# Kernel tuning notes

Hardware: AMD Instinct MI355X
Metric: run time of the kernel (lower is better)

## Reference

```python
import jax, jax.numpy as jnp
import numpy as np

B, T, C, H = 8, 2048, 1024, 128  # batch, seq, n_embed, head_size


def setup_inputs() -> dict:
    key = jax.random.key(0)
    ks = jax.random.split(key, 7)
    s = 1.0 / np.sqrt(C)
    return {
        "x": jax.random.normal(ks[0], (B, T, C), dtype=jnp.float32),
        "Wq": jax.random.uniform(ks[1], (C, H), jnp.float32, -s, s),
        "bq": jax.random.uniform(ks[2], (H,), jnp.float32, -s, s),
        "Wk": jax.random.uniform(ks[3], (C, H), jnp.float32, -s, s),
        "bk": jax.random.uniform(ks[4], (H,), jnp.float32, -s, s),
        "Wv": jax.random.uniform(ks[5], (C, H), jnp.float32, -s, s),
        "bv": jax.random.uniform(ks[6], (H,), jnp.float32, -s, s),
    }


def reference(x, Wq, bq, Wk, bk, Wv, bv):
    # Projections: [B, T, H]
    Q = jnp.einsum("btc,ch->bth", x, Wq) + bq
    K = jnp.einsum("btc,ch->bth", x, Wk) + bk
    V = jnp.einsum("btc,ch->bth", x, Wv) + bv
    # Scores scaled by n_embed**-0.5 (faithful to source, which uses C not head_size)
    scale = jnp.asarray(C, x.dtype) ** -0.5
    scores = jnp.einsum("bqh,bkh->bqk", Q, K) * scale  # [B, T, T]
    causal = jnp.tril(jnp.ones((T, T), dtype=bool))
    scores = jnp.where(causal, scores, jnp.asarray(-jnp.inf, x.dtype))
    attn = jax.nn.softmax(scores, axis=-1)
    # dropout p=0.0 (eval) -> identity
    return jnp.einsum("bqk,bkh->bqh", attn, V)
```

## Files before the change

kernel.cpp:

```cpp
#include <hip/hip_runtime.h>
#include <hip/hip_bf16.h>
#include <math.h>

typedef __attribute__((ext_vector_type(4))) float f32x4;
typedef __attribute__((ext_vector_type(8))) short s16x8;
typedef __attribute__((ext_vector_type(4))) short s16x4;

#define NB 8
#define NT 2048
#define NC 1024
#define NH 128
#define QSCALE 0.04508422002778f

__device__ __forceinline__ short f2bf(float f) {
  union { float f; unsigned u; } v; v.f = f;
  unsigned r = v.u + 0x7fffu + ((v.u >> 16) & 1u);
  return (short)(r >> 16);
}

__global__ void wt_kernel(const float* __restrict__ Wq, const float* __restrict__ Wk,
                          const float* __restrict__ Wv, short* __restrict__ Wt) {
  int idx = blockIdx.x * 256 + threadIdx.x;
  if (idx >= 3 * 128 * 1024) return;
  int m = idx >> 17;
  int n = (idx >> 10) & 127;
  int k = idx & 1023;
  const float* W = (m == 0) ? Wq : ((m == 1) ? Wk : Wv);
  Wt[idx] = f2bf(W[k * 128 + n]);
}

#define PK_PAD 72
#define PT_PAD 136

__global__ __launch_bounds__(256)
void proj_kernel(const float* __restrict__ x, const short* __restrict__ Wt,
                 const float* __restrict__ bq, const float* __restrict__ bk,
                 const float* __restrict__ bv,
                 short* __restrict__ Qb, short* __restrict__ Kb, short* __restrict__ Vtb) {
  __shared__ __align__(16) char smem[2 * 128 * PK_PAD * 2];
  short* Ax = (short*)smem;
  short* Bw = (short*)(smem + 128 * PK_PAD * 2);
  short* Tr = (short*)smem;

  const int tid = threadIdx.x;
  const int m0 = blockIdx.x * 128;
  const int proj = blockIdx.y;
  const int w = tid >> 6, lane = tid & 63;
  const int lr = lane & 15, lg = lane >> 4;

  f32x4 acc[2][8];
#pragma unroll
  for (int i = 0; i < 2; i++)
#pragma unroll
    for (int j = 0; j < 8; j++) acc[i][j] = {0.f, 0.f, 0.f, 0.f};

  const short* Wtp = Wt + proj * (128 * 1024);

  for (int k0 = 0; k0 < NC; k0 += 64) {
#pragma unroll
    for (int i = 0; i < 4; i++) {
      int idx = tid + 256 * i;
      int row = idx >> 3, c8 = idx & 7;
      const float* src = x + (size_t)(m0 + row) * NC + k0 + c8 * 8;
      float4 a = *(const float4*)src;
      float4 b = *(const float4*)(src + 4);
      s16x8 v;
      v[0] = f2bf(a.x); v[1] = f2bf(a.y); v[2] = f2bf(a.z); v[3] = f2bf(a.w);
      v[4] = f2bf(b.x); v[5] = f2bf(b.y); v[6] = f2bf(b.z); v[7] = f2bf(b.w);
      *(s16x8*)(Ax + row * PK_PAD + c8 * 8) = v;
    }
#pragma unroll
    for (int i = 0; i < 4; i++) {
      int idx = tid + 256 * i;
      int n = idx >> 3, c8 = idx & 7;
      s16x8 v = *(const s16x8*)(Wtp + n * 1024 + k0 + c8 * 8);
      *(s16x8*)(Bw + n * PK_PAD + c8 * 8) = v;
    }
    __syncthreads();
#pragma unroll
    for (int kc = 0; kc < 2; kc++) {
      s16x8 af[2];
#pragma unroll
      for (int mi = 0; mi < 2; mi++) {
        int row = w * 32 + mi * 16 + lr;
        af[mi] = *(const s16x8*)(Ax + row * PK_PAD + kc * 32 + lg * 8);
      }
#pragma unroll
      for (int ni = 0; ni < 8; ni++) {
        s16x8 bf = *(const s16x8*)(Bw + (ni * 16 + lr) * PK_PAD + kc * 32 + lg * 8);
        acc[0][ni] = __builtin_amdgcn_mfma_f32_16x16x32_bf16(af[0], bf, acc[0][ni], 0, 0, 0);
        acc[1][ni] = __builtin_amdgcn_mfma_f32_16x16x32_bf16(af[1], bf, acc[1][ni], 0, 0, 0);
      }
    }
    __syncthreads();
  }

  const float* bias = (proj == 0) ? bq : ((proj == 1) ? bk : bv);
  const float scl = (proj == 0) ? QSCALE : 1.0f;

  if (proj < 2) {
#pragma unroll
    for (int mi = 0; mi < 2; mi++)
#pragma unroll
      for (int ni = 0; ni < 8; ni++) {
        float bn = bias[ni * 16 + lr];
#pragma unroll
        for (int r = 0; r < 4; r++) {
          int t = w * 32 + mi * 16 + lg * 4 + r;
          Tr[t * PT_PAD + ni * 16 + lr] = f2bf((acc[mi][ni][r] + bn) * scl);
        }
      }
    __syncthreads();
    short* dst = (proj == 0) ? Qb : Kb;
#pragma unroll
    for (int i = 0; i < 8; i++) {
      int c = tid + 256 * i;
      int t = c >> 4, c8 = c & 15;
      s16x8 v = *(const s16x8*)(Tr + t * PT_PAD + c8 * 8);
      *(s16x8*)(dst + (size_t)(m0 + t) * NH + c8 * 8) = v;
    }
  } else {
#pragma unroll
    for (int mi = 0; mi < 2; mi++)
#pragma unroll
      for (int ni = 0; ni < 8; ni++) {
        float bn = bias[ni * 16 + lr];
        int d = ni * 16 + lr;
        int t = w * 32 + mi * 16 + lg * 4;
        s16x4 v;
        v[0] = f2bf(acc[mi][ni][0] + bn);
        v[1] = f2bf(acc[mi][ni][1] + bn);
        v[2] = f2bf(acc[mi][ni][2] + bn);
        v[3] = f2bf(acc[mi][ni][3] + bn);
        *(s16x4*)(Tr + d * PT_PAD + t) = v;
      }
    __syncthreads();
    int b = m0 >> 11;
    int tb = m0 & 2047;
#pragma unroll
    for (int i = 0; i < 8; i++) {
      int c = tid + 256 * i;
      int d = c >> 4, c8 = c & 15;
      s16x8 v = *(const s16x8*)(Tr + d * PT_PAD + c8 * 8);
      *(s16x8*)(Vtb + (size_t)b * (NH * NT) + (size_t)d * NT + tb + c8 * 8) = v;
    }
  }
}

#define KPAD 136
#define VPAD 72

__global__ __launch_bounds__(128)
void attn_kernel(const short* __restrict__ Qb, const short* __restrict__ Kb,
                 const short* __restrict__ Vtb, float* __restrict__ out) {
  __shared__ __align__(16) short Kl[64 * KPAD];
  __shared__ __align__(16) short Vl[128 * VPAD];

  const int tid = threadIdx.x;
  const int w = tid >> 6, lane = tid & 63;
  const int lr = lane & 15, lg = lane >> 4;

  const int bid = blockIdx.x;
  const int batch = bid >> 6;
  const int qtile = 63 - (bid & 63);
  const int q0 = qtile * 32;

  const int qrow = q0 + w * 16 + lr;
  const short* Qrow = Qb + (size_t)(batch * NT + qrow) * NH;
  s16x8 qf[4];
#pragma unroll
  for (int dc = 0; dc < 4; dc++) qf[dc] = *(const s16x8*)(Qrow + dc * 32 + lg * 8);

  f32x4 acc[8];
#pragma unroll
  for (int i = 0; i < 8; i++) acc[i] = {0.f, 0.f, 0.f, 0.f};
  float m_run = -3.0e38f, l_run = 0.f;

  const int ntiles = (q0 + 95) >> 6;
  const short* Kbase = Kb + (size_t)batch * NT * NH;
  const short* Vbase = Vtb + (size_t)batch * NH * NT;

  for (int it = 0; it < ntiles; it++) {
    const int kv0 = it * 64;
#pragma unroll
    for (int i = 0; i < 8; i++) {
      int idx = tid + 128 * i;
      int row = idx >> 4, c8 = idx & 15;
      s16x8 v = *(const s16x8*)(Kbase + (size_t)(kv0 + row) * NH + c8 * 8);
      *(s16x8*)(Kl + row * KPAD + c8 * 8) = v;
    }
#pragma unroll
    for (int i = 0; i < 8; i++) {
      int idx = tid + 128 * i;
      int d = idx >> 3, c8 = idx & 7;
      s16x8 v = *(const s16x8*)(Vbase + (size_t)d * NT + kv0 + c8 * 8);
      *(s16x8*)(Vl + d * VPAD + c8 * 8) = v;
    }
    __syncthreads();

    f32x4 st[4];
#pragma unroll
    for (int km = 0; km < 4; km++) st[km] = {0.f, 0.f, 0.f, 0.f};
#pragma unroll
    for (int dc = 0; dc < 4; dc++)
#pragma unroll
      for (int km = 0; km < 4; km++) {
        s16x8 kf = *(const s16x8*)(Kl + (km * 16 + lr) * KPAD + dc * 32 + lg * 8);
        st[km] = __builtin_amdgcn_mfma_f32_16x16x32_bf16(kf, qf[dc], st[km], 0, 0, 0);
      }

    if (kv0 + 63 > q0) {
#pragma unroll
      for (int km = 0; km < 4; km++)
#pragma unroll
        for (int r = 0; r < 4; r++) {
          int kg = kv0 + km * 16 + lg * 4 + r;
          if (kg > qrow) st[km][r] = -3.0e38f;
        }
    }

    float tm = -3.0e38f;
#pragma unroll
    for (int km = 0; km < 4; km++)
#pragma unroll
      for (int r = 0; r < 4; r++) tm = fmaxf(tm, st[km][r]);
    tm = fmaxf(tm, __shfl_xor(tm, 16, 64));
    tm = fmaxf(tm, __shfl_xor(tm, 32, 64));
    float m_new = fmaxf(m_run, tm);
    float corr = exp2f(m_run - m_new);

    float psum = 0.f;
    s16x8 pf[2];
#pragma unroll
    for (int km = 0; km < 4; km++)
#pragma unroll
      for (int r = 0; r < 4; r++) {
        float p = exp2f(st[km][r] - m_new);
        psum += p;
        pf[km >> 1][(km & 1) * 4 + r] = f2bf(p);
      }
    psum += __shfl_xor(psum, 16, 64);
    psum += __shfl_xor(psum, 32, 64);
    l_run = l_run * corr + psum;
    m_run = m_new;
#pragma unroll
    for (int i = 0; i < 8; i++) acc[i] *= corr;

#pragma unroll
    for (int ks = 0; ks < 2; ks++)
#pragma unroll
      for (int dm = 0; dm < 8; dm++) {
        const short* vp = Vl + (dm * 16 + lr) * VPAD + ks * 32 + lg * 4;
        s16x4 v0 = *(const s16x4*)vp;
        s16x4 v1 = *(const s16x4*)(vp + 16);
        s16x8 vf = __builtin_shufflevector(v0, v1, 0, 1, 2, 3, 4, 5, 6, 7);
        acc[dm] = __builtin_amdgcn_mfma_f32_16x16x32_bf16(vf, pf[ks], acc[dm], 0, 0, 0);
      }
    __syncthreads();
  }

  const float inv = 1.f / l_run;
  float* orow = out + (size_t)(batch * NT + qrow) * NH;
#pragma unroll
  for (int dm = 0; dm < 8; dm++) {
    float4 o;
    o.x = acc[dm][0] * inv;
    o.y = acc[dm][1] * inv;
    o.z = acc[dm][2] * inv;
    o.w = acc[dm][3] * inv;
    *(float4*)(orow + dm * 16 + lg * 4) = o;
  }
}

extern "C" void kernel_launch(void* const* d_in, const int* in_sizes, int n_in,
                              void* d_out, int out_size, void* d_ws, size_t ws_size,
                              hipStream_t stream) {
  const float* x = (const float*)d_in[0];
  const float* Wq = (const float*)d_in[1];
  const float* bq = (const float*)d_in[2];
  const float* Wk = (const float*)d_in[3];
  const float* bk = (const float*)d_in[4];
  const float* Wv = (const float*)d_in[5];
  const float* bv = (const float*)d_in[6];
  float* out = (float*)d_out;

  char* ws = (char*)d_ws;
  short* Wt = (short*)ws;
  short* Qb = (short*)(ws + 786432);
  short* Kb = (short*)(ws + 786432 + 4194304);
  short* Vtb = (short*)(ws + 786432 + 2 * 4194304);

  wt_kernel<<<dim3(1536), dim3(256), 0, stream>>>(Wq, Wk, Wv, Wt);
  proj_kernel<<<dim3(128, 3), dim3(256), 0, stream>>>(x, Wt, bq, bk, bv, Qb, Kb, Vtb);
  attn_kernel<<<dim3(512), dim3(128), 0, stream>>>(Qb, Kb, Vtb, out);
}
```

Before: 191.1 us.

## Rewrite all three kernels: tiled weight transpose, pipelined projection, split-KV attention

```diff
diff --git a/kernel.cpp b/kernel.cpp
--- a/kernel.cpp
+++ b/kernel.cpp
@@ -18,257 +18,284 @@
   return (short)(r >> 16);
 }
 
-__global__ void wt_kernel(const float* __restrict__ Wq, const float* __restrict__ Wk,
-                          const float* __restrict__ Wv, short* __restrict__ Wt) {
-  int idx = blockIdx.x * 256 + threadIdx.x;
-  if (idx >= 3 * 128 * 1024) return;
-  int m = idx >> 17;
-  int n = (idx >> 10) & 127;
-  int k = idx & 1023;
-  const float* W = (m == 0) ? Wq : ((m == 1) ? Wk : Wv);
-  Wt[idx] = f2bf(W[k * 128 + n]);
-}
-
-#define PK_PAD 72
-#define PT_PAD 136
+__device__ __forceinline__ void glds16(const short* g, short* l) {
+  __builtin_amdgcn_global_load_lds(
+      (const __attribute__((address_space(1))) unsigned int*)g,
+      (__attribute__((address_space(3))) unsigned int*)l, 16, 0, 0);
+}
 
 __global__ __launch_bounds__(256)
+void wt_kernel(const float* __restrict__ Wq, const float* __restrict__ Wk,
+               const float* __restrict__ Wv, short* __restrict__ Wt) {
+  __shared__ short T[64 * 72];
+  const int tid = threadIdx.x;
+  const int k0 = blockIdx.x * 64, n0 = blockIdx.y * 64, proj = blockIdx.z;
+  const float* W = (proj == 0) ? Wq : ((proj == 1) ? Wk : Wv);
+#pragma unroll
+  for (int u = 0; u < 4; u++) {
+    int row = u * 16 + (tid >> 4);
+    int col4 = (tid & 15) * 4;
+    float4 v = *(const float4*)(W + (size_t)(k0 + row) * NH + n0 + col4);
+    T[(col4 + 0) * 72 + row] = f2bf(v.x);
+    T[(col4 + 1) * 72 + row] = f2bf(v.y);
+    T[(col4 + 2) * 72 + row] = f2bf(v.z);
+    T[(col4 + 3) * 72 + row] = f2bf(v.w);
+  }
+  __syncthreads();
+#pragma unroll
+  for (int u = 0; u < 2; u++) {
+    int c = tid + 256 * u;
+    int n = c >> 3, c8 = c & 7;
+    s16x8 v = *(const s16x8*)(T + n * 72 + c8 * 8);
+    *(s16x8*)(Wt + (size_t)proj * (NH * NC) + (size_t)(n0 + n) * NC + k0 + c8 * 8) = v;
+  }
+}
+
+__global__ __launch_bounds__(256, 3)
 void proj_kernel(const float* __restrict__ x, const short* __restrict__ Wt,
                  const float* __restrict__ bq, const float* __restrict__ bk,
                  const float* __restrict__ bv,
                  short* __restrict__ Qb, short* __restrict__ Kb, short* __restrict__ Vtb) {
-  __shared__ __align__(16) char smem[2 * 128 * PK_PAD * 2];
-  short* Ax = (short*)smem;
-  short* Bw = (short*)(smem + 128 * PK_PAD * 2);
-  short* Tr = (short*)smem;
-
-  const int tid = threadIdx.x;
-  const int m0 = blockIdx.x * 128;
-  const int proj = blockIdx.y;
-  const int w = tid >> 6, lane = tid & 63;
-  const int lr = lane & 15, lg = lane >> 4;
-
-  f32x4 acc[2][8];
-#pragma unroll
-  for (int i = 0; i < 2; i++)
-#pragma unroll
-    for (int j = 0; j < 8; j++) acc[i][j] = {0.f, 0.f, 0.f, 0.f};
-
-  const short* Wtp = Wt + proj * (128 * 1024);
-
-  for (int k0 = 0; k0 < NC; k0 += 64) {
-#pragma unroll
-    for (int i = 0; i < 4; i++) {
-      int idx = tid + 256 * i;
-      int row = idx >> 3, c8 = idx & 7;
-      const float* src = x + (size_t)(m0 + row) * NC + k0 + c8 * 8;
-      float4 a = *(const float4*)src;
-      float4 b = *(const float4*)(src + 4);
-      s16x8 v;
-      v[0] = f2bf(a.x); v[1] = f2bf(a.y); v[2] = f2bf(a.z); v[3] = f2bf(a.w);
-      v[4] = f2bf(b.x); v[5] = f2bf(b.y); v[6] = f2bf(b.z); v[7] = f2bf(b.w);
-      *(s16x8*)(Ax + row * PK_PAD + c8 * 8) = v;
-    }
-#pragma unroll
-    for (int i = 0; i < 4; i++) {
-      int idx = tid + 256 * i;
-      int n = idx >> 3, c8 = idx & 7;
-      s16x8 v = *(const s16x8*)(Wtp + n * 1024 + k0 + c8 * 8);
-      *(s16x8*)(Bw + n * PK_PAD + c8 * 8) = v;
-    }
-    __syncthreads();
-#pragma unroll
-    for (int kc = 0; kc < 2; kc++) {
-      s16x8 af[2];
-#pragma unroll
-      for (int mi = 0; mi < 2; mi++) {
-        int row = w * 32 + mi * 16 + lr;
-        af[mi] = *(const s16x8*)(Ax + row * PK_PAD + kc * 32 + lg * 8);
-      }
-#pragma unroll
-      for (int ni = 0; ni < 8; ni++) {
-        s16x8 bf = *(const s16x8*)(Bw + (ni * 16 + lr) * PK_PAD + kc * 32 + lg * 8);
-        acc[0][ni] = __builtin_amdgcn_mfma_f32_16x16x32_bf16(af[0], bf, acc[0][ni], 0, 0, 0);
-        acc[1][ni] = __builtin_amdgcn_mfma_f32_16x16x32_bf16(af[1], bf, acc[1][ni], 0, 0, 0);
-      }
-    }
-    __syncthreads();
-  }
-
-  const float* bias = (proj == 0) ? bq : ((proj == 1) ? bk : bv);
-  const float scl = (proj == 0) ? QSCALE : 1.0f;
-
-  if (proj < 2) {
-#pragma unroll
-    for (int mi = 0; mi < 2; mi++)
-#pragma unroll
-      for (int ni = 0; ni < 8; ni++) {
-        float bn = bias[ni * 16 + lr];
-#pragma unroll
-        for (int r = 0; r < 4; r++) {
-          int t = w * 32 + mi * 16 + lg * 4 + r;
-          Tr[t * PT_PAD + ni * 16 + lr] = f2bf((acc[mi][ni][r] + bn) * scl);
-        }
-      }
-    __syncthreads();
-    short* dst = (proj == 0) ? Qb : Kb;
-#pragma unroll
-    for (int i = 0; i < 8; i++) {
-      int c = tid + 256 * i;
-      int t = c >> 4, c8 = c & 15;
-      s16x8 v = *(const s16x8*)(Tr + t * PT_PAD + c8 * 8);
-      *(s16x8*)(dst + (size_t)(m0 + t) * NH + c8 * 8) = v;
-    }
-  } else {
-#pragma unroll
-    for (int mi = 0; mi < 2; mi++)
-#pragma unroll
-      for (int ni = 0; ni < 8; ni++) {
-        float bn = bias[ni * 16 + lr];
-        int d = ni * 16 + lr;
-        int t = w * 32 + mi * 16 + lg * 4;
-        s16x4 v;
-        v[0] = f2bf(acc[mi][ni][0] + bn);
-        v[1] = f2bf(acc[mi][ni][1] + bn);
-        v[2] = f2bf(acc[mi][ni][2] + bn);
-        v[3] = f2bf(acc[mi][ni][3] + bn);
-        *(s16x4*)(Tr + d * PT_PAD + t) = v;
-      }
-    __syncthreads();
-    int b = m0 >> 11;
-    int tb = m0 & 2047;
-#pragma unroll
-    for (int i = 0; i < 8; i++) {
-      int c = tid + 256 * i;
-      int d = c >> 4, c8 = c & 15;
-      s16x8 v = *(const s16x8*)(Tr + d * PT_PAD + c8 * 8);
-      *(s16x8*)(Vtb + (size_t)b * (NH * NT) + (size_t)d * NT + tb + c8 * 8) = v;
-    }
-  }
-}
-
-#define KPAD 136
-#define VPAD 72
-
-__global__ __launch_bounds__(128)
-void attn_kernel(const short* __restrict__ Qb, const short* __restrict__ Kb,
-                 const short* __restrict__ Vtb, float* __restrict__ out) {
-  __shared__ __align__(16) short Kl[64 * KPAD];
-  __shared__ __align__(16) short Vl[128 * VPAD];
+  __shared__ __align__(16) short smem[2 * 12288];
 
   const int tid = threadIdx.x;
   const int w = tid >> 6, lane = tid & 63;
   const int lr = lane & 15, lg = lane >> 4;
 
   const int bid = blockIdx.x;
-  const int batch = bid >> 6;
-  const int qtile = 63 - (bid & 63);
-  const int q0 = qtile * 32;
-
-  const int qrow = q0 + w * 16 + lr;
-  const short* Qrow = Qb + (size_t)(batch * NT + qrow) * NH;
-  s16x8 qf[4];
-#pragma unroll
-  for (int dc = 0; dc < 4; dc++) qf[dc] = *(const s16x8*)(Qrow + dc * 32 + lg * 8);
+  const int orig = (bid & 7) * 96 + (bid >> 3);
+  const int proj = orig >> 8;
+  const int m0 = (orig & 255) * 64;
+
+  const short* Wtp = Wt + (size_t)proj * (NH * NC);
 
   f32x4 acc[8];
 #pragma unroll
   for (int i = 0; i < 8; i++) acc[i] = {0.f, 0.f, 0.f, 0.f};
-  float m_run = -3.0e38f, l_run = 0.f;
-
-  const int ntiles = (q0 + 95) >> 6;
-  const short* Kbase = Kb + (size_t)batch * NT * NH;
-  const short* Vbase = Vtb + (size_t)batch * NH * NT;
-
-  for (int it = 0; it < ntiles; it++) {
-    const int kv0 = it * 64;
-#pragma unroll
-    for (int i = 0; i < 8; i++) {
-      int idx = tid + 128 * i;
-      int row = idx >> 4, c8 = idx & 15;
-      s16x8 v = *(const s16x8*)(Kbase + (size_t)(kv0 + row) * NH + c8 * 8);
-      *(s16x8*)(Kl + row * KPAD + c8 * 8) = v;
-    }
-#pragma unroll
-    for (int i = 0; i < 8; i++) {
-      int idx = tid + 128 * i;
-      int d = idx >> 3, c8 = idx & 7;
-      s16x8 v = *(const s16x8*)(Vbase + (size_t)d * NT + kv0 + c8 * 8);
-      *(s16x8*)(Vl + d * VPAD + c8 * 8) = v;
-    }
-    __syncthreads();
-
-    f32x4 st[4];
-#pragma unroll
-    for (int km = 0; km < 4; km++) st[km] = {0.f, 0.f, 0.f, 0.f};
-#pragma unroll
-    for (int dc = 0; dc < 4; dc++)
-#pragma unroll
-      for (int km = 0; km < 4; km++) {
-        s16x8 kf = *(const s16x8*)(Kl + (km * 16 + lr) * KPAD + dc * 32 + lg * 8);
-        st[km] = __builtin_amdgcn_mfma_f32_16x16x32_bf16(kf, qf[dc], st[km], 0, 0, 0);
-      }
-
-    if (kv0 + 63 > q0) {
-#pragma unroll
-      for (int km = 0; km < 4; km++)
+
+  const int s0 = 2 * tid, s1 = 2 * tid + 1;
+  const int ar0 = s0 >> 3, ac0 = s0 & 7, ar1 = s1 >> 3, ac1 = s1 & 7;
+  const float* asrc0base = x + (size_t)(m0 + ar0) * NC + ((ac0 ^ (ar0 & 7)) * 8);
+  const float* asrc1base = x + (size_t)(m0 + ar1) * NC + ((ac1 ^ (ar1 & 7)) * 8);
+
+  float4 a00, a01, a10, a11;
+
+  auto stageA_load = [&](int k0) {
+    a00 = *(const float4*)(asrc0base + k0);
+    a01 = *(const float4*)(asrc0base + k0 + 4);
+    a10 = *(const float4*)(asrc1base + k0);
+    a11 = *(const float4*)(asrc1base + k0 + 4);
+  };
+  auto stageA_write = [&](int buf) {
+    s16x8 v;
+    v[0] = f2bf(a00.x); v[1] = f2bf(a00.y); v[2] = f2bf(a00.z); v[3] = f2bf(a00.w);
+    v[4] = f2bf(a01.x); v[5] = f2bf(a01.y); v[6] = f2bf(a01.z); v[7] = f2bf(a01.w);
+    *(s16x8*)(smem + buf * 12288 + s0 * 8) = v;
+    v[0] = f2bf(a10.x); v[1] = f2bf(a10.y); v[2] = f2bf(a10.z); v[3] = f2bf(a10.w);
+    v[4] = f2bf(a11.x); v[5] = f2bf(a11.y); v[6] = f2bf(a11.z); v[7] = f2bf(a11.w);
+    *(s16x8*)(smem + buf * 12288 + s1 * 8) = v;
+  };
+  auto stageB = [&](int buf, int k0) {
+#pragma unroll
+    for (int u = 0; u < 4; u++) {
+      int g = w * 4 + u;
+      int s = g * 64 + lane;
+      int n = s >> 3, c8 = s & 7;
+      const short* src = Wtp + (size_t)n * NC + k0 + ((c8 ^ (n & 7)) * 8);
+      short* dst = smem + buf * 12288 + 4096 + g * 512;
+      glds16(src, dst);
+    }
+  };
+
+  stageA_load(0);
+  stageB(0, 0);
+  stageA_write(0);
+  __syncthreads();
+
+  for (int it = 0; it < 16; ++it) {
+    int buf = it & 1, nb = buf ^ 1;
+    if (it < 15) { stageA_load((it + 1) * 64); stageB(nb, (it + 1) * 64); }
+    const short* A = smem + buf * 12288;
+    const short* B = smem + buf * 12288 + 4096;
+    const int arow = w * 16 + lr;
+#pragma unroll
+    for (int kc = 0; kc < 2; kc++) {
+      s16x8 af = *(const s16x8*)(A + arow * 64 + (((kc * 4 + lg) ^ (arow & 7)) * 8));
+#pragma unroll
+      for (int ni = 0; ni < 8; ni++) {
+        int brow = ni * 16 + lr;
+        s16x8 bf = *(const s16x8*)(B + brow * 64 + (((kc * 4 + lg) ^ (brow & 7)) * 8));
+        acc[ni] = __builtin_amdgcn_mfma_f32_16x16x32_bf16(af, bf, acc[ni], 0, 0, 0);
+      }
+    }
+    if (it < 15) stageA_write(nb);
+    __syncthreads();
+  }
+
+  const float* bias = (proj == 0) ? bq : ((proj == 1) ? bk : bv);
+  const float scl = (proj == 0) ? QSCALE : 1.0f;
+  short* Tr = smem;
+
+  if (proj < 2) {
+#pragma unroll
+    for (int ni = 0; ni < 8; ni++) {
+      float bn = bias[ni * 16 + lr];
+#pragma unroll
+      for (int r = 0; r < 4; r++) {
+        int t = w * 16 + lg * 4 + r;
+        Tr[t * 136 + ni * 16 + lr] = f2bf((acc[ni][r] + bn) * scl);
+      }
+    }
+    __syncthreads();
+    short* dst = (proj == 0) ? Qb : Kb;
+#pragma unroll
+    for (int i = 0; i < 4; i++) {
+      int c = tid + 256 * i;
+      int t = c >> 4, c8 = c & 15;
+      s16x8 v = *(const s16x8*)(Tr + t * 136 + c8 * 8);
+      *(s16x8*)(dst + (size_t)(m0 + t) * NH + c8 * 8) = v;
+    }
+  } else {
+#pragma unroll
+    for (int ni = 0; ni < 8; ni++) {
+      float bn = bias[ni * 16 + lr];
+      int d = ni * 16 + lr;
+      int t = w * 16 + lg * 4;
+      s16x4 v;
+      v[0] = f2bf(acc[ni][0] + bn);
+      v[1] = f2bf(acc[ni][1] + bn);
+      v[2] = f2bf(acc[ni][2] + bn);
+      v[3] = f2bf(acc[ni][3] + bn);
+      *(s16x4*)(Tr + d * 72 + t) = v;
+    }
+    __syncthreads();
+    int b = m0 >> 11, t0 = m0 & 2047;
+#pragma unroll
+    for (int i = 0; i < 4; i++) {
+      int c = tid + 256 * i;
+      int d = c >> 3, c8 = c & 7;
+      s16x8 v = *(const s16x8*)(Tr + d * 72 + c8 * 8);
+      *(s16x8*)(Vtb + (size_t)b * (NH * NT) + (size_t)d * NT + t0 + c8 * 8) = v;
+    }
+  }
+}
+
+__global__ __launch_bounds__(256, 3)
+void attn_kernel(const short* __restrict__ Qb, const short* __restrict__ Kb,
+                 const short* __restrict__ Vtb, float* __restrict__ out) {
+  __shared__ float Cb[3][16][132];
+  __shared__ float2 Ml[3][16];
+
+  const int tid = threadIdx.x;
+  const int w = tid >> 6, lane = tid & 63;
+  const int lr = lane & 15, lg = lane >> 4;
+
+  const int bid = blockIdx.x;
+  const int orig = (bid & 7) * 64 + (bid >> 3);
+  const int batch = orig >> 6;
+  const int pairid = orig & 63;
+
+  const short* Kp = Kb + (size_t)batch * NT * NH;
+  const short* Vp = Vtb + (size_t)batch * NH * NT;
+
+#pragma unroll 1
+  for (int ph = 0; ph < 2; ph++) {
+    const int j = ph ? (127 - pairid) : pairid;
+    const int q0 = j * 16;
+    const int q = q0 + lr;
+
+    const short* Qrow = Qb + (size_t)(batch * NT + q) * NH;
+    s16x8 qf[4];
+#pragma unroll
+    for (int dc = 0; dc < 4; dc++) qf[dc] = *(const s16x8*)(Qrow + dc * 32 + lg * 8);
+
+    f32x4 acc[8];
+#pragma unroll
+    for (int i = 0; i < 8; i++) acc[i] = {0.f, 0.f, 0.f, 0.f};
+    float m_run = -3.0e38f, l_run = 0.f;
+
+    const int Nt = (q0 + 47) >> 5;
+
+    for (int t = w; t < Nt; t += 4) {
+      const int kv0 = t * 32;
+      f32x4 st0 = {0.f, 0.f, 0.f, 0.f}, st1 = st0;
+      const short* Kt = Kp + (size_t)(kv0 + lr) * NH + lg * 8;
+#pragma unroll
+      for (int dc = 0; dc < 4; dc++) {
+        s16x8 k0f = *(const s16x8*)(Kt + dc * 32);
+        s16x8 k1f = *(const s16x8*)(Kt + 16 * NH + dc * 32);
+        st0 = __builtin_amdgcn_mfma_f32_16x16x32_bf16(k0f, qf[dc], st0, 0, 0, 0);
+        st1 = __builtin_amdgcn_mfma_f32_16x16x32_bf16(k1f, qf[dc], st1, 0, 0, 0);
+      }
+      if (kv0 + 31 > q0) {
 #pragma unroll
         for (int r = 0; r < 4; r++) {
-          int kg = kv0 + km * 16 + lg * 4 + r;
-          if (kg > qrow) st[km][r] = -3.0e38f;
+          if (kv0 + lg * 4 + r > q) st0[r] = -3.0e38f;
+          if (kv0 + 16 + lg * 4 + r > q) st1[r] = -3.0e38f;
         }
-    }
-
-    float tm = -3.0e38f;
-#pragma unroll
-    for (int km = 0; km < 4; km++)
-#pragma unroll
-      for (int r = 0; r < 4; r++) tm = fmaxf(tm, st[km][r]);
-    tm = fmaxf(tm, __shfl_xor(tm, 16, 64));
-    tm = fmaxf(tm, __shfl_xor(tm, 32, 64));
-    float m_new = fmaxf(m_run, tm);
-    float corr = exp2f(m_run - m_new);
-
-    float psum = 0.f;
-    s16x8 pf[2];
-#pragma unroll
-    for (int km = 0; km < 4; km++)
+      }
+      float tm = -3.0e38f;
+#pragma unroll
+      for (int r = 0; r < 4; r++) { tm = fmaxf(tm, st0[r]); tm = fmaxf(tm, st1[r]); }
+      tm = fmaxf(tm, __shfl_xor(tm, 16, 64));
+      tm = fmaxf(tm, __shfl_xor(tm, 32, 64));
+      float m_new = fmaxf(m_run, tm);
+      float corr = exp2f(m_run - m_new);
+      float psum = 0.f;
+      s16x8 pf;
 #pragma unroll
       for (int r = 0; r < 4; r++) {
-        float p = exp2f(st[km][r] - m_new);
-        psum += p;
-        pf[km >> 1][(km & 1) * 4 + r] = f2bf(p);
-      }
-    psum += __shfl_xor(psum, 16, 64);
-    psum += __shfl_xor(psum, 32, 64);
-    l_run = l_run * corr + psum;
-    m_run = m_new;
-#pragma unroll
-    for (int i = 0; i < 8; i++) acc[i] *= corr;
-
-#pragma unroll
-    for (int ks = 0; ks < 2; ks++)
+        float p0 = exp2f(st0[r] - m_new);
+        float p1 = exp2f(st1[r] - m_new);
+        psum += p0 + p1;
+        pf[r] = f2bf(p0);
+        pf[4 + r] = f2bf(p1);
+      }
+      psum += __shfl_xor(psum, 16, 64);
+      psum += __shfl_xor(psum, 32, 64);
+      l_run = l_run * corr + psum;
+      m_run = m_new;
+#pragma unroll
+      for (int i = 0; i < 8; i++) acc[i] *= corr;
 #pragma unroll
       for (int dm = 0; dm < 8; dm++) {
-        const short* vp = Vl + (dm * 16 + lr) * VPAD + ks * 32 + lg * 4;
+        const short* vp = Vp + (size_t)(dm * 16 + lr) * NT + kv0 + lg * 4;
         s16x4 v0 = *(const s16x4*)vp;
         s16x4 v1 = *(const s16x4*)(vp + 16);
         s16x8 vf = __builtin_shufflevector(v0, v1, 0, 1, 2, 3, 4, 5, 6, 7);
-        acc[dm] = __builtin_amdgcn_mfma_f32_16x16x32_bf16(vf, pf[ks], acc[dm], 0, 0, 0);
-      }
-    __syncthreads();
-  }
-
-  const float inv = 1.f / l_run;
-  float* orow = out + (size_t)(batch * NT + qrow) * NH;
-#pragma unroll
-  for (int dm = 0; dm < 8; dm++) {
-    float4 o;
-    o.x = acc[dm][0] * inv;
-    o.y = acc[dm][1] * inv;
-    o.z = acc[dm][2] * inv;
-    o.w = acc[dm][3] * inv;
-    *(float4*)(orow + dm * 16 + lg * 4) = o;
+        acc[dm] = __builtin_amdgcn_mfma_f32_16x16x32_bf16(vf, pf, acc[dm], 0, 0, 0);
+      }
+    }
+
+    __syncthreads();
+    if (w > 0) {
+#pragma unroll
+      for (int dm = 0; dm < 8; dm++)
+        *(f32x4*)&Cb[w - 1][lr][dm * 16 + lg * 4] = acc[dm];
+      if (lg == 0) Ml[w - 1][lr] = make_float2(m_run, l_run);
+    }
+    __syncthreads();
+    if (w == 0) {
+      float2 ml0 = Ml[0][lr], ml1 = Ml[1][lr], ml2 = Ml[2][lr];
+      float M = fmaxf(fmaxf(m_run, ml0.x), fmaxf(ml1.x, ml2.x));
+      float c0 = exp2f(m_run - M);
+      float c1 = exp2f(ml0.x - M);
+      float c2 = exp2f(ml1.x - M);
+      float c3 = exp2f(ml2.x - M);
+      float lt = l_run * c0 + ml0.y * c1 + ml1.y * c2 + ml2.y * c3;
+      float inv = 1.0f / lt;
+      float* orow = out + (size_t)(batch * NT + q) * NH;
+#pragma unroll
+      for (int dm = 0; dm < 8; dm++) {
+        f32x4 v = acc[dm] * c0;
+        v += (*(const f32x4*)&Cb[0][lr][dm * 16 + lg * 4]) * c1;
+        v += (*(const f32x4*)&Cb[1][lr][dm * 16 + lg * 4]) * c2;
+        v += (*(const f32x4*)&Cb[2][lr][dm * 16 + lg * 4]) * c3;
+        v *= inv;
+        *(f32x4*)(orow + dm * 16 + lg * 4) = v;
+      }
+    }
+    __syncthreads();
   }
 }
 
@@ -290,7 +317,7 @@
   short* Kb = (short*)(ws + 786432 + 4194304);
   short* Vtb = (short*)(ws + 786432 + 2 * 4194304);
 
-  wt_kernel<<<dim3(1536), dim3(256), 0, stream>>>(Wq, Wk, Wv, Wt);
-  proj_kernel<<<dim3(128, 3), dim3(256), 0, stream>>>(x, Wt, bq, bk, bv, Qb, Kb, Vtb);
-  attn_kernel<<<dim3(512), dim3(128), 0, stream>>>(Qb, Kb, Vtb, out);
-}
+  wt_kernel<<<dim3(16, 2, 3), dim3(256), 0, stream>>>(Wq, Wk, Wv, Wt);
+  proj_kernel<<<dim3(768), dim3(256), 0, stream>>>(x, Wt, bq, bk, bv, Qb, Kb, Vtb);
+  attn_kernel<<<dim3(512), dim3(256), 0, stream>>>(Qb, Kb, Vtb, out);
+}
```

Measured after the change: 221.4 us. +15.9%, slower.
